# Kernel tuning notes

Hardware: AMD Instinct MI355X
Metric: run time of the kernel (lower is better)

Reference implementation:

```python
import jax, jax.numpy as jnp
import numpy as np
import math

K = 3          # kernel_size
P_GEM = 3.0    # GeM power
EPS_GEM = 1e-6
EPS_NORM = 1e-12


def _l2n(x, axis):
    n = jnp.sqrt(jnp.sum(x * x, axis=axis, keepdims=True))
    return x / jnp.maximum(n, EPS_NORM)


def setup_inputs() -> dict:
    key = jax.random.key(0)
    ks = jax.random.split(key, 7)
    b, hw, c, nc = 32, 196, 768, 4096
    hidden = c  # mlp_ratio = 1
    return {
        "patch_tokens": jax.random.normal(ks[0], (b, hw, c), dtype=jnp.float32),
        "fc1_w": jax.random.normal(ks[1], (c, hidden), dtype=jnp.float32) * 0.02,
        "fc1_b": jnp.zeros((hidden,), dtype=jnp.float32),
        "fc2_w": jax.random.normal(ks[2], (hidden, c), dtype=jnp.float32) * 0.02,
        "fc2_b": jnp.zeros((c,), dtype=jnp.float32),
        "head_w": jax.random.normal(ks[3], (c, nc), dtype=jnp.float32) * 0.02,
        "head_b": jnp.zeros((nc,), dtype=jnp.float32),
    }


def reference(patch_tokens, fc1_w, fc1_b, fc2_w, fc2_b, head_w, head_b):
    b, hw, c = patch_tokens.shape
    h = w = int(math.sqrt(hw))

    # ---- SpaceSelfAware: pad -> unfold (3x3 local windows) -> multiply ----
    img = jnp.transpose(patch_tokens, (0, 2, 1)).reshape(b, c, h, w)
    # ZeroPad2d((left=1, right=1, top=2, bottom=0)) for kernel_size=3
    padded = jnp.pad(img, ((0, 0), (0, 0), (K - 1, 0), (K // 2, K // 2)))
    # stack the 9 shifted views, row-major over (ki, kj) matching nn.Unfold
    wins = jnp.stack(
        [padded[:, :, ki:ki + h, kj:kj + w] for ki in range(K) for kj in range(K)],
        axis=2,
    )  # (b, c, 9, h, w)
    y = wins.reshape(b, c, K, K, hw)
    y = jnp.transpose(y, (0, 4, 1, 2, 3))  # (b, hw, c, K, K)
    ssa = patch_tokens[:, :, :, None, None] * y  # (b, hw, c, K, K)

    # ---- space_fusion: L2Norm(dim=1) then GeM(p=3) over the KxK window ----
    ssa = _l2n(ssa, axis=1)
    pooled = jnp.mean(jnp.clip(ssa, EPS_GEM, None) ** P_GEM, axis=(-2, -1)) ** (1.0 / P_GEM)  # (b, hw, c)

    # ---- residual + L2 normalize over channels + Mlp ----
    tokens = pooled + patch_tokens
    tokens = _l2n(tokens, axis=-1)
    hdn = jax.nn.gelu(tokens @ fc1_w + fc1_b, approximate=False)
    tokens = hdn @ fc2_w + fc2_b  # (b, hw, c)

    # ---- GeMHead: GeM(p=3) over tokens, linear to nc, L2 normalize ----
    g = jnp.mean(jnp.clip(tokens, EPS_GEM, None) ** P_GEM, axis=1) ** (1.0 / P_GEM)  # (b, c)
    desc = g @ head_w + head_b  # (b, nc)
    desc = _l2n(desc, axis=-1)
    return desc
```

## Files before the change

kernel.cpp:

```cpp
#include <hip/hip_runtime.h>
#include <hip/hip_bf16.h>
#include <math.h>

#define B   32
#define P   196
#define C   768
#define NC  4096
#define HH  14
#define KSPLIT 24
#define NT  12
#define M6  6272
#define TW  (768 * 32)
#define TM  (M6 * 32)

typedef _Float16 half8 __attribute__((ext_vector_type(8)));
typedef _Float16 half4 __attribute__((ext_vector_type(4)));
typedef float f32x4 __attribute__((ext_vector_type(4)));

#define GLOAD_LDS16(g, l)                                                      \
    __builtin_amdgcn_global_load_lds(                                          \
        (const __attribute__((address_space(1))) void*)(g),                    \
        (__attribute__((address_space(3))) void*)(l), 16, 0, 0)

__global__ __launch_bounds__(256) void k_ssa(const float* __restrict__ t,
                                             _Float16* __restrict__ outP,
                                             float* __restrict__ partial) {
    const int b = blockIdx.y, cb = blockIdx.x, c0 = cb * 16;
    __shared__ float xp_[256 * 16];
    __shared__ float part[4][9][16];
    __shared__ float inv_norm[9][16];
    __shared__ _Float16 outT[P][16];
    const int tid = threadIdx.x;
    const int cc = tid & 15, g = tid >> 4, wv = tid >> 6;

#pragma unroll
    for (int q = 0; q < 16; ++q) xp_[q * 256 + tid] = 0.0f;
    __syncthreads();

    for (int idx = tid; idx < 784; idx += 256) {
        const int p = idx >> 2, c = (idx & 3) * 4;
        const int i = p / HH, j = p % HH;
        *(float4*)&xp_[((i + 2) * 16 + (j + 1)) * 16 + c] =
            *(const float4*)&t[((size_t)b * P + p) * C + c0 + c];
    }
    __syncthreads();

    float s[9] = {};
    {
        int i = 0, j = g;
        if (j >= HH) { j -= HH; i = 1; }
        for (int p = g; p < P; p += 16) {
            const int base = ((i + 2) * 16 + (j + 1)) * 16 + cc;
            const float xp = xp_[base];
            const float xp2 = xp * xp;
#pragma unroll
            for (int k = 0; k < 9; ++k) {
                const int off = ((k / 3) - 2) * 16 + (k % 3) - 1;
                const float nb = xp_[base + off * 16];
                s[k] += xp2 * nb * nb;
            }
            j += 2; ++i;
            if (j >= HH) { j -= HH; ++i; }
        }
    }
#pragma unroll
    for (int k = 0; k < 9; ++k) {
        float r = s[k];
        r += __shfl_xor(r, 16);
        r += __shfl_xor(r, 32);
        s[k] = r;
    }
    if ((tid & 63) < 16) {
#pragma unroll
        for (int k = 0; k < 9; ++k) part[wv][k][cc] = s[k];
    }
    __syncthreads();
    if (tid < 144) {
        const int k = tid >> 4, c2 = tid & 15;
        const float t4 = part[0][k][c2] + part[1][k][c2] +
                         part[2][k][c2] + part[3][k][c2];
        inv_norm[k][c2] = 1.0f / fmaxf(sqrtf(t4), 1e-12f);
    }
    __syncthreads();

    float invn[9];
#pragma unroll
    for (int k = 0; k < 9; ++k) invn[k] = inv_norm[k][cc];

    {
        int i = 0, j = g;
        if (j >= HH) { j -= HH; i = 1; }
        for (int p = g; p < P; p += 16) {
            const int base = ((i + 2) * 16 + (j + 1)) * 16 + cc;
            const float xp = xp_[base];
            float acc = 0.0f;
#pragma unroll
            for (int k = 0; k < 9; ++k) {
                const int off = ((k / 3) - 2) * 16 + (k % 3) - 1;
                const float v = xp * xp_[base + off * 16];
                const float u = fmaxf(v * invn[k], 1e-6f);
                acc += u * u * u;
            }
            const float val = cbrtf(acc * (1.0f / 9.0f)) + xp;
            float rs = val * val;
            rs += __shfl_xor(rs, 1);
            rs += __shfl_xor(rs, 2);
            rs += __shfl_xor(rs, 4);
            rs += __shfl_xor(rs, 8);
            outT[p][cc] = (_Float16)val;
            if (cc == 0) partial[(size_t)cb * M6 + b * P + p] = rs;
            j += 2; ++i;
            if (j >= HH) { j -= HH; ++i; }
        }
    }
    __syncthreads();
    const int kb = cb >> 1, kbase = (cb & 1) * 16;
    for (int idx = tid; idx < P * 2; idx += 256) {
        const int p = idx >> 1, h = idx & 1;
        const half8 v = *(const half8*)&outT[p][h * 8];
        const int row = b * P + p;
        const int slot = ((kbase + h * 8) >> 3) ^ ((row >> 1) & 3);
        *(half8*)&outP[(size_t)kb * TM + (size_t)row * 32 + slot * 8] = v;
    }
}

__global__ __launch_bounds__(256) void k_inv(const float* __restrict__ partial,
                                             float* __restrict__ inv) {
    const int row = blockIdx.x * 256 + threadIdx.x;
    if (row < M6) {
        float s = 0.0f;
#pragma unroll 8
        for (int cb = 0; cb < 48; ++cb) s += partial[(size_t)cb * M6 + row];
        inv[row] = 1.0f / fmaxf(sqrtf(s), 1e-12f);
    }
}

__global__ __launch_bounds__(256) void k_wt(const float* __restrict__ W1,
                                            const float* __restrict__ W2,
                                            _Float16* __restrict__ O1,
                                            _Float16* __restrict__ O2) {
    const float* W = blockIdx.z ? W2 : W1;
    _Float16* WtP = blockIdx.z ? O2 : O1;
    __shared__ float tt[32][33];
    const int k0 = blockIdx.x * 32, n0 = blockIdx.y * 32;
    const int r = threadIdx.x / 32, c = threadIdx.x % 32;
#pragma unroll
    for (int q = 0; q < 4; ++q)
        tt[r + q * 8][c] = W[(size_t)(k0 + r + q * 8) * C + n0 + c];
    __syncthreads();
    const int nl = threadIdx.x >> 3, h = threadIdx.x & 7;
    const int n = n0 + nl;
    half4 v;
#pragma unroll
    for (int j = 0; j < 4; ++j) v[j] = (_Float16)tt[h * 4 + j][nl];
    const int el = (h * 4) ^ (((n >> 1) & 3) << 3);
    *(half4*)&WtP[(size_t)blockIdx.x * TW + (size_t)n * 32 + el] = v;
}

template <bool GELU>
__global__ __launch_bounds__(256) void k_mfma_gemm(
    const _Float16* __restrict__ TokP,
    const _Float16* __restrict__ WtP,
    const float* __restrict__ bias,
    const float* __restrict__ invv,
    _Float16* __restrict__ Cout) {
    __shared__ _Float16 lA[3][2][64][32];
    __shared__ _Float16 lB[3][2][64][32];
    const int tid = threadIdx.x;
    const int w = tid >> 6, l = tid & 63;
    const int l15 = l & 15, lk = l >> 4;

    const int lid = blockIdx.x;
    int vm, vn;
    if (lid < 1152) { vm = (lid / 96) * 8 + (lid & 7); vn = (lid % 96) >> 3; }
    else            { const int r = lid - 1152; vm = 96 + r / 12; vn = r % 12; }
    const int m0 = vm * 64, n0 = vn * 64;
    const int wn = (w & 1) * 32, wm = (w >> 1) * 32;

    f32x4 acc[2][2] = {};

    const int kbsel = w & 1;
    const bool isB = (w >= 2);
    const _Float16* srcBase =
        isB ? (TokP + (size_t)m0 * 32) : (WtP + (size_t)n0 * 32);
    const size_t tileStride = isB ? (size_t)TM : (size_t)TW;
    _Float16* dst0 = isB ? &lB[0][kbsel][0][0] : &lA[0][kbsel][0][0];

#define ISSUE(tt, bf_)                                                         \
    {   const _Float16* s_ = srcBase + (size_t)(2 * (tt) + kbsel) * tileStride;\
        _Float16* d_ = dst0 + (size_t)(bf_) * 4096;                            \
        GLOAD_LDS16(s_ + l * 8,        d_ + l * 8);                            \
        GLOAD_LDS16(s_ + 512 + l * 8,  d_ + 512 + l * 8);                      \
        GLOAD_LDS16(s_ + 1024 + l * 8, d_ + 1024 + l * 8);                     \
        GLOAD_LDS16(s_ + 1536 + l * 8, d_ + 1536 + l * 8); }

    ISSUE(0, 0); ISSUE(1, 1); ISSUE(2, 2);

    for (int t = 0; t < NT; ++t) {
        if (t < NT - 2)       asm volatile("s_waitcnt vmcnt(8)" ::: "memory");
        else if (t == NT - 2) asm volatile("s_waitcnt vmcnt(4)" ::: "memory");
        else                  asm volatile("s_waitcnt vmcnt(0)" ::: "memory");
        __builtin_amdgcn_s_barrier();
        __builtin_amdgcn_sched_barrier(0);

        const int buf = t % 3;
#pragma unroll
        for (int kk = 0; kk < 2; ++kk) {
            half8 af[2], bf[2];
#pragma unroll
            for (int fa = 0; fa < 2; ++fa) {
                const int rowA = wn + fa * 16 + l15;
                const int colA = (lk ^ ((rowA >> 1) & 3)) * 8;
                af[fa] = *(const half8*)&lA[buf][kk][rowA][colA];
            }
#pragma unroll
            for (int fb = 0; fb < 2; ++fb) {
                const int rowB = wm + fb * 16 + l15;
                const int colB = (lk ^ ((rowB >> 1) & 3)) * 8;
                bf[fb] = *(const half8*)&lB[buf][kk][rowB][colB];
            }
#pragma unroll
            for (int fa = 0; fa < 2; ++fa)
#pragma unroll
                for (int fb = 0; fb < 2; ++fb)
                    acc[fa][fb] = __builtin_amdgcn_mfma_f32_16x16x32_f16(
                        af[fa], bf[fb], acc[fa][fb], 0, 0, 0);
        }
        asm volatile("s_waitcnt lgkmcnt(0)" ::: "memory");
        __builtin_amdgcn_s_barrier();
        __builtin_amdgcn_sched_barrier(0);
        if (t < NT - 3) ISSUE(t + 3, buf);
    }
#undef ISSUE

    float invm[2];
    if (GELU) {
#pragma unroll
        for (int fb = 0; fb < 2; ++fb)
            invm[fb] = invv[m0 + wm + fb * 16 + l15];
    }
#pragma unroll
    for (int fa = 0; fa < 2; ++fa) {
        const int nb = n0 + wn + fa * 16 + lk * 4;
        const float4 bv = *(const float4*)&bias[nb];
#pragma unroll
        for (int fb = 0; fb < 2; ++fb) {
            const int m = m0 + wm + fb * 16 + l15;
            half4 o;
            if (GELU) {
#pragma unroll
                for (int rr = 0; rr < 4; ++rr) {
                    float v = acc[fa][fb][rr] * invm[fb] + ((const float*)&bv)[rr];
                    v = 0.5f * v * (1.0f + erff(v * 0.70710678118654752f));
                    o[rr] = (_Float16)v;
                }
                const int el = (nb & 31) ^ (((m >> 1) & 3) << 3);
                *(half4*)&Cout[(size_t)(nb >> 5) * TM + (size_t)m * 32 + el] = o;
            } else {
#pragma unroll
                for (int rr = 0; rr < 4; ++rr)
                    o[rr] = (_Float16)(acc[fa][fb][rr] + ((const float*)&bv)[rr]);
                *(half4*)&Cout[(size_t)m * C + nb] = o;
            }
        }
    }
}

__global__ __launch_bounds__(256) void k_gempool(const _Float16* __restrict__ tk,
                                                 float* __restrict__ g) {
    const int b = blockIdx.x / 12;
    const int c0 = (blockIdx.x % 12) * 64;
    const int tid = threadIdx.x;
    const int cc = tid & 63, pg = tid >> 6;
    float s = 0.0f;
    for (int p = pg * 49; p < pg * 49 + 49; ++p) {
        const float v = fmaxf((float)tk[((size_t)b * P + p) * C + c0 + cc], 1e-6f);
        s += v * v * v;
    }
    __shared__ float part[4][64];
    part[pg][cc] = s;
    __syncthreads();
    if (tid < 64) {
        const float t4 = part[0][cc] + part[1][cc] + part[2][cc] + part[3][cc];
        g[b * C + c0 + cc] = cbrtf(t4 * (1.0f / (float)P));
    }
}

__global__ __launch_bounds__(256) void k_head1(const float* __restrict__ g,
                                               const float* __restrict__ W,
                                               float* __restrict__ partial) {
    const int n0 = blockIdx.x * 64;
    const int k0 = blockIdx.y * 32;
    __shared__ float gs[32][32];
    __shared__ float part[4][32][64];
    const int tid = threadIdx.x;

    for (int idx = tid; idx < 32 * 32; idx += 256)
        gs[idx >> 5][idx & 31] = g[(idx >> 5) * C + k0 + (idx & 31)];
    __syncthreads();

    const int c = tid & 63, q = tid >> 6;
    float acc[32] = {};
#pragma unroll
    for (int kk = 0; kk < 8; ++kk) {
        const int k = q * 8 + kk;
        const float wv = W[(size_t)(k0 + k) * NC + n0 + c];
#pragma unroll
        for (int b = 0; b < 32; ++b) acc[b] += gs[b][k] * wv;
    }
#pragma unroll
    for (int b = 0; b < 32; ++b) part[q][b][c] = acc[b];
    __syncthreads();

    for (int o = tid; o < 32 * 64; o += 256) {
        const int b = o >> 6, cc = o & 63;
        const float v = part[0][b][cc] + part[1][b][cc] +
                        part[2][b][cc] + part[3][b][cc];
        partial[((size_t)blockIdx.y * 32 + b) * NC + n0 + cc] = v;
    }
}

__global__ __launch_bounds__(256) void k_head2(const float* __restrict__ partial,
                                               const float* __restrict__ hb,
                                               float* __restrict__ out) {
    const int n = blockIdx.x * 256 + threadIdx.x;
    const int b = blockIdx.y;
    float s = hb[n];
#pragma unroll
    for (int ks = 0; ks < KSPLIT; ++ks)
        s += partial[((size_t)ks * 32 + b) * NC + n];
    out[(size_t)b * NC + n] = s;
}

__global__ __launch_bounds__(256) void k_outnorm(float* __restrict__ out) {
    const int b = blockIdx.x;
    float* r = out + (size_t)b * NC;
    const int tid = threadIdx.x;
    float v[16];
    float s = 0.0f;
#pragma unroll
    for (int q = 0; q < 16; ++q) {
        v[q] = r[tid + q * 256];
        s += v[q] * v[q];
    }
    __shared__ float partial[4];
    __shared__ float inv;
#pragma unroll
    for (int off = 32; off > 0; off >>= 1) s += __shfl_xor(s, off);
    if ((tid & 63) == 0) partial[tid >> 6] = s;
    __syncthreads();
    if (tid == 0)
        inv = 1.0f / fmaxf(sqrtf(partial[0] + partial[1] + partial[2] + partial[3]), 1e-12f);
    __syncthreads();
#pragma unroll
    for (int q = 0; q < 16; ++q) r[tid + q * 256] = v[q] * inv;
}

extern "C" void kernel_launch(void* const* d_in, const int* in_sizes, int n_in,
                              void* d_out, int out_size, void* d_ws, size_t ws_size,
                              hipStream_t stream) {
    const float* patch  = (const float*)d_in[0];
    const float* fc1_w  = (const float*)d_in[1];
    const float* fc1_b  = (const float*)d_in[2];
    const float* fc2_w  = (const float*)d_in[3];
    const float* fc2_b  = (const float*)d_in[4];
    const float* head_w = (const float*)d_in[5];
    const float* head_b = (const float*)d_in[6];
    float* out = (float*)d_out;

    const size_t big = (size_t)B * P * C;
    _Float16* tokU  = (_Float16*)d_ws;
    _Float16* hdnP  = tokU + big;
    _Float16* wt1   = hdnP + big;
    _Float16* wt2   = wt1 + C * C;
    float*    spart = (float*)(wt2 + C * C);
    float*    invv  = spart + 48 * (size_t)M6;
    float*    gbuf  = invv + M6;
    float*    hpart = gbuf + B * C;
    _Float16* tok2  = (_Float16*)(hpart + (size_t)KSPLIT * 32 * NC);

    k_ssa<<<dim3(48, B), dim3(256), 0, stream>>>(patch, tokU, spart);
    k_inv<<<dim3((M6 + 255) / 256), dim3(256), 0, stream>>>(spart, invv);
    k_wt<<<dim3(C / 32, C / 32, 2), dim3(256), 0, stream>>>(
        fc1_w, fc2_w, wt1, wt2);
    k_mfma_gemm<true><<<dim3(1176), dim3(256), 0, stream>>>(
        tokU, wt1, fc1_b, invv, hdnP);
    k_mfma_gemm<false><<<dim3(1176), dim3(256), 0, stream>>>(
        hdnP, wt2, fc2_b, nullptr, tok2);
    k_gempool<<<dim3(B * 12), dim3(256), 0, stream>>>(tok2, gbuf);
    k_head1<<<dim3(NC / 64, KSPLIT), dim3(256), 0, stream>>>(gbuf, head_w, hpart);
    k_head2<<<dim3(NC / 256, B), dim3(256), 0, stream>>>(hpart, head_b, out);
    k_outnorm<<<dim3(B), dim3(256), 0, stream>>>(out);
}
```

Before: 93.31 us.

## Fuse GeM token pooling into fc2 GEMM epilogue and merge prep kernels

The fc2 GEMM epilogue now computes clamped cubes per output tile and reduces them per batch segment into a small partial buffer, so the full fp16 token tensor is never written and re-read by a separate pooling kernel. A tiny kernel sums the four partials and takes the cube root. The inverse-norm kernel is merged into the weight-transpose launch as an extra z-slice to save a launch, and the head GEMV split-K factor is halved with larger K tiles. The cost is extra shuffle reductions and a block barrier in the GEMM epilogue, plus tile-to-batch boundary bookkeeping that must be correct.

```diff
diff --git a/kernel.cpp b/kernel.cpp
--- a/kernel.cpp
+++ b/kernel.cpp
@@ -7,7 +7,7 @@
 #define C   768
 #define NC  4096
 #define HH  14
-#define KSPLIT 24
+#define KSPLIT 12
 #define NT  12
 #define M6  6272
 #define TW  (768 * 32)
@@ -124,21 +124,22 @@
     }
 }
 
-__global__ __launch_bounds__(256) void k_inv(const float* __restrict__ partial,
-                                             float* __restrict__ inv) {
-    const int row = blockIdx.x * 256 + threadIdx.x;
-    if (row < M6) {
-        float s = 0.0f;
+__global__ __launch_bounds__(256) void k_prep(const float* __restrict__ W1,
+                                              const float* __restrict__ W2,
+                                              _Float16* __restrict__ O1,
+                                              _Float16* __restrict__ O2,
+                                              const float* __restrict__ spart,
+                                              float* __restrict__ invv) {
+    if (blockIdx.z == 2) {
+        const int row = (blockIdx.y * 24 + blockIdx.x) * 256 + threadIdx.x;
+        if (row < M6) {
+            float s = 0.0f;
 #pragma unroll 8
-        for (int cb = 0; cb < 48; ++cb) s += partial[(size_t)cb * M6 + row];
-        inv[row] = 1.0f / fmaxf(sqrtf(s), 1e-12f);
-    }
-}
-
-__global__ __launch_bounds__(256) void k_wt(const float* __restrict__ W1,
-                                            const float* __restrict__ W2,
-                                            _Float16* __restrict__ O1,
-                                            _Float16* __restrict__ O2) {
+            for (int cb = 0; cb < 48; ++cb) s += spart[(size_t)cb * M6 + row];
+            invv[row] = 1.0f / fmaxf(sqrtf(s), 1e-12f);
+        }
+        return;
+    }
     const float* W = blockIdx.z ? W2 : W1;
     _Float16* WtP = blockIdx.z ? O2 : O1;
     __shared__ float tt[32][33];
@@ -163,9 +164,11 @@
     const _Float16* __restrict__ WtP,
     const float* __restrict__ bias,
     const float* __restrict__ invv,
-    _Float16* __restrict__ Cout) {
+    _Float16* __restrict__ Cout,
+    float* __restrict__ gpart) {
     __shared__ _Float16 lA[3][2][64][32];
     __shared__ _Float16 lB[3][2][64][32];
+    __shared__ float part2[2][2][64];
     const int tid = threadIdx.x;
     const int w = tid >> 6, l = tid & 63;
     const int l15 = l & 15, lk = l >> 4;
@@ -233,8 +236,10 @@
     }
 #undef ISSUE
 
+    const int b0 = m0 / P;
+    const int rsplit = (b0 + 1) * P;
     float invm[2];
-    if (GELU) {
+    if constexpr (GELU) {
 #pragma unroll
         for (int fb = 0; fb < 2; ++fb)
             invm[fb] = invv[m0 + wm + fb * 16 + l15];
@@ -243,11 +248,11 @@
     for (int fa = 0; fa < 2; ++fa) {
         const int nb = n0 + wn + fa * 16 + lk * 4;
         const float4 bv = *(const float4*)&bias[nb];
-#pragma unroll
-        for (int fb = 0; fb < 2; ++fb) {
-            const int m = m0 + wm + fb * 16 + l15;
-            half4 o;
-            if (GELU) {
+        if constexpr (GELU) {
+#pragma unroll
+            for (int fb = 0; fb < 2; ++fb) {
+                const int m = m0 + wm + fb * 16 + l15;
+                half4 o;
 #pragma unroll
                 for (int rr = 0; rr < 4; ++rr) {
                     float v = acc[fa][fb][rr] * invm[fb] + ((const float*)&bv)[rr];
@@ -256,54 +261,74 @@
                 }
                 const int el = (nb & 31) ^ (((m >> 1) & 3) << 3);
                 *(half4*)&Cout[(size_t)(nb >> 5) * TM + (size_t)m * 32 + el] = o;
-            } else {
-#pragma unroll
-                for (int rr = 0; rr < 4; ++rr)
-                    o[rr] = (_Float16)(acc[fa][fb][rr] + ((const float*)&bv)[rr]);
-                *(half4*)&Cout[(size_t)m * C + nb] = o;
-            }
-        }
-    }
-}
-
-__global__ __launch_bounds__(256) void k_gempool(const _Float16* __restrict__ tk,
-                                                 float* __restrict__ g) {
-    const int b = blockIdx.x / 12;
-    const int c0 = (blockIdx.x % 12) * 64;
-    const int tid = threadIdx.x;
-    const int cc = tid & 63, pg = tid >> 6;
-    float s = 0.0f;
-    for (int p = pg * 49; p < pg * 49 + 49; ++p) {
-        const float v = fmaxf((float)tk[((size_t)b * P + p) * C + c0 + cc], 1e-6f);
-        s += v * v * v;
-    }
-    __shared__ float part[4][64];
-    part[pg][cc] = s;
-    __syncthreads();
-    if (tid < 64) {
-        const float t4 = part[0][cc] + part[1][cc] + part[2][cc] + part[3][cc];
-        g[b * C + c0 + cc] = cbrtf(t4 * (1.0f / (float)P));
-    }
+            }
+        } else {
+#pragma unroll
+            for (int rr = 0; rr < 4; ++rr) {
+                float s0 = 0.0f, s1 = 0.0f;
+#pragma unroll
+                for (int fb = 0; fb < 2; ++fb) {
+                    const int m = m0 + wm + fb * 16 + l15;
+                    const float v = acc[fa][fb][rr] + ((const float*)&bv)[rr];
+                    const float u = fmaxf(v, 1e-6f);
+                    const float u3 = u * u * u;
+                    if (m >= rsplit) s1 += u3; else s0 += u3;
+                }
+                s0 += __shfl_xor(s0, 1); s0 += __shfl_xor(s0, 2);
+                s0 += __shfl_xor(s0, 4); s0 += __shfl_xor(s0, 8);
+                s1 += __shfl_xor(s1, 1); s1 += __shfl_xor(s1, 2);
+                s1 += __shfl_xor(s1, 4); s1 += __shfl_xor(s1, 8);
+                if (l15 == 0) {
+                    part2[w >> 1][0][wn + fa * 16 + lk * 4 + rr] = s0;
+                    part2[w >> 1][1][wn + fa * 16 + lk * 4 + rr] = s1;
+                }
+            }
+        }
+    }
+    if constexpr (!GELU) {
+        __syncthreads();
+        if (tid < 128) {
+            const int seg = tid >> 6, nn = tid & 63;
+            const float tot = part2[0][seg][nn] + part2[1][seg][nn];
+            if (seg == 0) {
+                const int q = vm - ((b0 * 49) >> 4);
+                gpart[((size_t)b0 * 4 + q) * C + n0 + nn] = tot;
+            } else if (rsplit < m0 + 64) {
+                gpart[((size_t)(b0 + 1) * 4 + 0) * C + n0 + nn] = tot;
+            }
+        }
+    }
+}
+
+__global__ __launch_bounds__(256) void k_gempool2(const float* __restrict__ gpart,
+                                                  float* __restrict__ g) {
+    const int b = blockIdx.x / 3;
+    const int c = (blockIdx.x % 3) * 256 + threadIdx.x;
+    const float s = gpart[((size_t)b * 4 + 0) * C + c] +
+                    gpart[((size_t)b * 4 + 1) * C + c] +
+                    gpart[((size_t)b * 4 + 2) * C + c] +
+                    gpart[((size_t)b * 4 + 3) * C + c];
+    g[b * C + c] = cbrtf(s * (1.0f / (float)P));
 }
 
 __global__ __launch_bounds__(256) void k_head1(const float* __restrict__ g,
                                                const float* __restrict__ W,
                                                float* __restrict__ partial) {
     const int n0 = blockIdx.x * 64;
-    const int k0 = blockIdx.y * 32;
-    __shared__ float gs[32][32];
+    const int k0 = blockIdx.y * 64;
+    __shared__ float gs[32][64];
     __shared__ float part[4][32][64];
     const int tid = threadIdx.x;
 
-    for (int idx = tid; idx < 32 * 32; idx += 256)
-        gs[idx >> 5][idx & 31] = g[(idx >> 5) * C + k0 + (idx & 31)];
+    for (int idx = tid; idx < 32 * 64; idx += 256)
+        gs[idx >> 6][idx & 63] = g[(idx >> 6) * C + k0 + (idx & 63)];
     __syncthreads();
 
     const int c = tid & 63, q = tid >> 6;
     float acc[32] = {};
 #pragma unroll
-    for (int kk = 0; kk < 8; ++kk) {
-        const int k = q * 8 + kk;
+    for (int kk = 0; kk < 16; ++kk) {
+        const int k = q * 16 + kk;
         const float wv = W[(size_t)(k0 + k) * NC + n0 + c];
 #pragma unroll
         for (int b = 0; b < 32; ++b) acc[b] += gs[b][k] * wv;
@@ -376,18 +401,17 @@
     float*    spart = (float*)(wt2 + C * C);
     float*    invv  = spart + 48 * (size_t)M6;
     float*    gbuf  = invv + M6;
-    float*    hpart = gbuf + B * C;
-    _Float16* tok2  = (_Float16*)(hpart + (size_t)KSPLIT * 32 * NC);
+    float*    gpart = gbuf + B * C;
+    float*    hpart = gpart + (size_t)B * 4 * C;
 
     k_ssa<<<dim3(48, B), dim3(256), 0, stream>>>(patch, tokU, spart);
-    k_inv<<<dim3((M6 + 255) / 256), dim3(256), 0, stream>>>(spart, invv);
-    k_wt<<<dim3(C / 32, C / 32, 2), dim3(256), 0, stream>>>(
-        fc1_w, fc2_w, wt1, wt2);
+    k_prep<<<dim3(C / 32, C / 32, 3), dim3(256), 0, stream>>>(
+        fc1_w, fc2_w, wt1, wt2, spart, invv);
     k_mfma_gemm<true><<<dim3(1176), dim3(256), 0, stream>>>(
-        tokU, wt1, fc1_b, invv, hdnP);
+        tokU, wt1, fc1_b, invv, hdnP, nullptr);
     k_mfma_gemm<false><<<dim3(1176), dim3(256), 0, stream>>>(
-        hdnP, wt2, fc2_b, nullptr, tok2);
-    k_gempool<<<dim3(B * 12), dim3(256), 0, stream>>>(tok2, gbuf);
+        hdnP, wt2, fc2_b, nullptr, nullptr, gpart);
+    k_gempool2<<<dim3(B * 3), dim3(256), 0, stream>>>(gpart, gbuf);
     k_head1<<<dim3(NC / 64, KSPLIT), dim3(256), 0, stream>>>(gbuf, head_w, hpart);
     k_head2<<<dim3(NC / 256, B), dim3(256), 0, stream>>>(hpart, head_b, out);
     k_outnorm<<<dim3(B), dim3(256), 0, stream>>>(out);
```

Result: faster. 82.59 us (-11.5%).
